# Performance work log

Measured on AMD Instinct MI355X. Metric: run time of the kernel, lower is better.

## Reference

```python
import jax, jax.numpy as jnp
import numpy as np

D_MODEL = 2048
NUM_HEADS = 16
HEAD_DIM = 128
BATCH = 4
SEQ = 2048


def setup_inputs() -> dict:
    key = jax.random.key(0)
    ks = jax.random.split(key, 5)
    s = 0.02
    return {
        "x": jax.random.normal(ks[0], (BATCH, SEQ, D_MODEL), dtype=jnp.float32),
        "Wq": jax.random.normal(ks[1], (NUM_HEADS * HEAD_DIM, D_MODEL), dtype=jnp.float32) * s,
        "Wk": jax.random.normal(ks[2], (NUM_HEADS * HEAD_DIM, D_MODEL), dtype=jnp.float32) * s,
        "Wv": jax.random.normal(ks[3], (NUM_HEADS * HEAD_DIM, D_MODEL), dtype=jnp.float32) * s,
        "Wo": jax.random.normal(ks[4], (D_MODEL, NUM_HEADS * HEAD_DIM), dtype=jnp.float32) * s,
    }


def _split_heads(t):
    b, s, _ = t.shape
    return t.reshape(b, s, NUM_HEADS, HEAD_DIM).transpose(0, 2, 1, 3)  # [b,h,s,d]


def reference(x, Wq, Wk, Wv, Wo):
    # prefill: QKV proj + causal SDPA + output proj. torch Linear: x @ W.T
    q = _split_heads(x @ Wq.T)
    k = _split_heads(x @ Wk.T)
    v = _split_heads(x @ Wv.T)
    scale = 1.0 / jnp.sqrt(jnp.asarray(HEAD_DIM, dtype=x.dtype))
    scores = jnp.einsum("bhqd,bhkd->bhqk", q, k) * scale
    causal = jnp.tril(jnp.ones((SEQ, SEQ), dtype=bool))
    scores = jnp.where(causal, scores, jnp.finfo(scores.dtype).min)
    attn = jax.nn.softmax(scores, axis=-1)
    y = jnp.einsum("bhqk,bhkd->bhqd", attn, v)
    y = y.transpose(0, 2, 1, 3).reshape(x.shape[0], SEQ, NUM_HEADS * HEAD_DIM)
    y = y @ Wo.T
    return (y, k, v)
```

## Files before the change

kernel.cpp:

```cpp
#include <hip/hip_runtime.h>
#include <stdint.h>

#define DM 2048
#define NH 16
#define HD 128
#define BB 4
#define SS 2048
#define BS (BB*SS)
#define NQKV (3*DM)
#define SCQ 0.12751744565f

typedef __bf16 bf16_t;
typedef __attribute__((ext_vector_type(8))) __bf16 bf16x8;
typedef __attribute__((ext_vector_type(4))) float f32x4;
typedef __attribute__((ext_vector_type(16))) float f32x16;
typedef __attribute__((ext_vector_type(4))) float float4v;
typedef __attribute__((ext_vector_type(4))) unsigned int uint4v;
typedef __attribute__((ext_vector_type(4))) unsigned short ushort4v;
typedef __attribute__((ext_vector_type(8))) unsigned short ushort8;

__device__ __forceinline__ unsigned short f2bf(float f) {
  unsigned u = __float_as_uint(f);
  u += 0x7fffu + ((u >> 16) & 1u);
  return (unsigned short)(u >> 16);
}

__device__ __forceinline__ void gl16(const void* g, void* l) {
  __builtin_amdgcn_global_load_lds(
      (const __attribute__((address_space(1))) unsigned int*)(unsigned long long)g,
      (__attribute__((address_space(3))) unsigned int*)(unsigned int)(unsigned long long)l,
      16, 0, 0);
}

#define DSR(dst, addr, IMM)                                                   \
  asm volatile("ds_read_b128 %0, %1 offset:" IMM : "=v"(dst) : "v"(addr))

__global__ void conv_all(const float* __restrict__ x,  const float* __restrict__ wq,
                         const float* __restrict__ wk, const float* __restrict__ wv,
                         const float* __restrict__ wo,
                         unsigned short* __restrict__ xbf,
                         unsigned short* __restrict__ wqkv,
                         unsigned short* __restrict__ wobf) {
  const int NX = BS * DM / 4;
  const int NW = DM * DM / 4;
  int i = blockIdx.x * blockDim.x + threadIdx.x;
  int stride = gridDim.x * blockDim.x;
  for (; i < NX + 4 * NW; i += stride) {
    const float4v* src;
    ushort4v* dst;
    if (i < NX)               { src = (const float4v*)x  + i;            dst = (ushort4v*)xbf + i; }
    else if (i < NX + NW)     { int j = i - NX;          src = (const float4v*)wq + j; dst = (ushort4v*)wqkv + j; }
    else if (i < NX + 2 * NW) { int j = i - NX - NW;     src = (const float4v*)wk + j; dst = (ushort4v*)wqkv + NW + j; }
    else if (i < NX + 3 * NW) { int j = i - NX - 2 * NW; src = (const float4v*)wv + j; dst = (ushort4v*)wqkv + 2 * NW + j; }
    else                      { int j = i - NX - 3 * NW; src = (const float4v*)wo + j; dst = (ushort4v*)wobf + j; }
    float4v v = *src;
    ushort4v o;
    o.x = f2bf(v.x); o.y = f2bf(v.y); o.z = f2bf(v.z); o.w = f2bf(v.w);
    *dst = o;
  }
}

__global__ void vtrans(const float* __restrict__ vf, bf16_t* __restrict__ vt) {
  __shared__ unsigned short T[128 * 64];
  const int t = threadIdx.x;
  const int s0 = blockIdx.x * 64;
  const int bh = blockIdx.y;
  const size_t in_off = (size_t)bh * SS * HD;
  const int sr = t >> 5, c4 = t & 31;
#pragma unroll
  for (int j = 0; j < 8; ++j) {
    int s = j * 8 + sr;
    float4v v = *(const float4v*)(vf + in_off + (size_t)(s0 + s) * HD + c4 * 4);
#pragma unroll
    for (int q = 0; q < 4; ++q) {
      int d = c4 * 4 + q;
      int bc = s * 2;
      int byt = d * 128 + ((((bc >> 4) ^ (d & 7)) << 4) | (bc & 15));
      *(unsigned short*)((char*)T + byt) = f2bf(v[q]);
    }
  }
  __syncthreads();
  const int dr = t >> 3, c8 = t & 7;
  unsigned short* out = (unsigned short*)vt + (size_t)bh * HD * SS;
#pragma unroll
  for (int j = 0; j < 4; ++j) {
    int d = j * 32 + dr;
    ushort8 val = *(const ushort8*)((char*)T + d * 128 + ((c8 ^ (d & 7)) << 4));
    *(ushort8*)(out + (size_t)d * SS + s0 + c8 * 8) = val;
  }
}

__global__ void gemmq(const bf16_t* __restrict__ A, const bf16_t* __restrict__ Bm,
                      bf16_t* __restrict__ qbf, bf16_t* __restrict__ kbt,
                      float* __restrict__ kf, float* __restrict__ vf) {
  __shared__ bf16_t As[128 * 64];
  __shared__ bf16_t Bs[128 * 64];
  const int t = threadIdx.x;
  const int w = t >> 6, lane = t & 63;
  const int wm = (w >> 1) * 64, wn = (w & 1) * 64;
  const int row0 = blockIdx.x * 128, col0 = blockIdx.y * 128;
  const int fr = lane & 15, fq = lane >> 4;
  const int K = DM;

  f32x4 acc[4][4] = {};

  for (int kk = 0; kk < K; kk += 64) {
    __syncthreads();
#pragma unroll
    for (int j = 0; j < 4; ++j) {
      int u = j * 256 + t;
      int r = u >> 3, c = u & 7;
      uint4v dA = *(const uint4v*)(A + (size_t)(row0 + r) * K + kk + c * 8);
      uint4v dB = *(const uint4v*)(Bm + (size_t)(col0 + r) * K + kk + c * 8);
      int so = r * 64 + ((c ^ ((r >> 1) & 7)) * 8);
      *(uint4v*)(As + so) = dA;
      *(uint4v*)(Bs + so) = dB;
    }
    __syncthreads();
#pragma unroll
    for (int ks = 0; ks < 2; ++ks) {
      bf16x8 af[4], bfv[4];
#pragma unroll
      for (int f = 0; f < 4; ++f) {
        int ra = wm + f * 16 + fr;
        af[f] = *(const bf16x8*)(As + ra * 64 + (((fq + ks * 4) ^ ((ra >> 1) & 7)) * 8));
        int rb = wn + f * 16 + fr;
        bfv[f] = *(const bf16x8*)(Bs + rb * 64 + (((fq + ks * 4) ^ ((rb >> 1) & 7)) * 8));
      }
#pragma unroll
      for (int i = 0; i < 4; ++i)
#pragma unroll
        for (int jn = 0; jn < 4; ++jn)
          acc[i][jn] = __builtin_amdgcn_mfma_f32_16x16x32_bf16(af[i], bfv[jn], acc[i][jn], 0, 0, 0);
    }
  }

#pragma unroll
  for (int i = 0; i < 4; ++i) {
#pragma unroll
    for (int jn = 0; jn < 4; ++jn) {
#pragma unroll
      for (int r = 0; r < 4; ++r) {
        int m = row0 + wm + i * 16 + fq * 4 + r;
        int n = col0 + wn + jn * 16 + fr;
        float v = acc[i][jn][r];
        int b = m >> 11, s = m & 2047;
        if (n < DM) {
          int h = n >> 7, d = n & 127;
          qbf[(((size_t)(b * NH + h)) * SS + s) * HD + d] = (bf16_t)(v * SCQ);
        } else if (n < 2 * DM) {
          int nn = n - DM, h = nn >> 7, d = nn & 127;
          size_t o = (((size_t)(b * NH + h)) * SS + s) * HD + d;
          kbt[o] = (bf16_t)v;
          kf[o] = v;
        } else {
          int nn = n - 2 * DM, h = nn >> 7, d = nn & 127;
          vf[(((size_t)(b * NH + h)) * SS + s) * HD + d] = v;
        }
      }
    }
  }
}

template<int MODE>
__global__ __launch_bounds__(512)
void gemmr4(const bf16_t* __restrict__ A, const bf16_t* __restrict__ Bm,
            const int K, const int N, const int nbx,
            float* __restrict__ Cf) {
  __shared__ bf16_t As[4][256 * 32];
  __shared__ bf16_t Bs[4][256 * 32];
  const int t = threadIdx.x, w = t >> 6, lane = t & 63;
  const int fr = lane & 15, fq = lane >> 4;
  const int cpx = gridDim.x >> 3;
  const int orig = blockIdx.x;
  const int wg = (orig & 7) * cpx + (orig >> 3);
  const int bm = wg % nbx, bn = wg / nbx;
  const int row0 = bm * 256, col0 = bn * 256;
  const int wm = (w >> 2) * 128, wn = (w & 3) * 64;

  const bf16_t* Asrc[2];
  const bf16_t* Bsrc[2];
  int dst[2];
#pragma unroll
  for (int j = 0; j < 2; ++j) {
    int u = j * 512 + t, r = u >> 2, c = u & 3;
    Asrc[j] = A + (size_t)(row0 + r) * K + ((c ^ ((r >> 1) & 3)) * 8);
    Bsrc[j] = Bm + (size_t)(col0 + r) * K + ((c ^ ((r >> 1) & 3)) * 8);
    dst[j] = u * 16;
  }
  const int NT = K >> 5;
  f32x4 acc[8][4] = {};

  const unsigned As0 = (unsigned)(unsigned long long)(const void*)&As[0][0];
  const unsigned Bs0 = (unsigned)(unsigned long long)(const void*)&Bs[0][0];
  const unsigned xorc = (unsigned)((fq ^ ((fr >> 1) & 3)) << 4);
  const unsigned aoff = (unsigned)((wm + fr) * 64) + xorc;
  const unsigned boff = (unsigned)((wn + fr) * 64) + xorc;

#define STAGE(TT)                                                  \
  {                                                                \
    const int sl_ = (TT) & 3;                                      \
    const size_t ko_ = (size_t)(TT) * 32;                          \
    gl16(Asrc[0] + ko_, (char*)(&As[sl_][0]) + dst[0]);            \
    gl16(Asrc[1] + ko_, (char*)(&As[sl_][0]) + dst[1]);            \
    gl16(Bsrc[0] + ko_, (char*)(&Bs[sl_][0]) + dst[0]);            \
    gl16(Bsrc[1] + ko_, (char*)(&Bs[sl_][0]) + dst[1]);            \
  }

#define MFQUAD(FI, AV)                                                        \
  acc[FI][0] = __builtin_amdgcn_mfma_f32_16x16x32_bf16(                       \
      __builtin_bit_cast(bf16x8, AV), __builtin_bit_cast(bf16x8, bv0), acc[FI][0], 0, 0, 0); \
  acc[FI][1] = __builtin_amdgcn_mfma_f32_16x16x32_bf16(                       \
      __builtin_bit_cast(bf16x8, AV), __builtin_bit_cast(bf16x8, bv1), acc[FI][1], 0, 0, 0); \
  acc[FI][2] = __builtin_amdgcn_mfma_f32_16x16x32_bf16(                       \
      __builtin_bit_cast(bf16x8, AV), __builtin_bit_cast(bf16x8, bv2), acc[FI][2], 0, 0, 0); \
  acc[FI][3] = __builtin_amdgcn_mfma_f32_16x16x32_bf16(                       \
      __builtin_bit_cast(bf16x8, AV), __builtin_bit_cast(bf16x8, bv3), acc[FI][3], 0, 0, 0);

  STAGE(0); STAGE(1); STAGE(2);

  for (int T = 0; T < NT; ++T) {
    if (T + 2 < NT) {
      asm volatile("s_waitcnt vmcnt(8)" ::: "memory");
    } else if (T + 1 < NT) {
      asm volatile("s_waitcnt vmcnt(4)" ::: "memory");
    } else {
      asm volatile("s_waitcnt vmcnt(0)" ::: "memory");
    }
    asm volatile("s_barrier" ::: "memory");
    if (T + 3 < NT) STAGE(T + 3);

    const unsigned ab = As0 + (unsigned)(T & 3) * 16384 + aoff;
    const unsigned bb = Bs0 + (unsigned)(T & 3) * 16384 + boff;
    uint4v bv0, bv1, bv2, bv3, a0, a1, a2, a3, a4, a5, a6, a7;
    DSR(bv0, bb, "0");    DSR(bv1, bb, "1024");
    DSR(bv2, bb, "2048"); DSR(bv3, bb, "3072");
    DSR(a0, ab, "0");     DSR(a1, ab, "1024");
    DSR(a2, ab, "2048");  DSR(a3, ab, "3072");
    DSR(a4, ab, "4096");  DSR(a5, ab, "5120");
    DSR(a6, ab, "6144");  DSR(a7, ab, "7168");

    asm volatile("s_waitcnt lgkmcnt(4)" ::: "memory");
    __builtin_amdgcn_sched_barrier(0);
    __builtin_amdgcn_s_setprio(1);
    MFQUAD(0, a0) MFQUAD(1, a1) MFQUAD(2, a2) MFQUAD(3, a3)
    __builtin_amdgcn_s_setprio(0);

    asm volatile("s_waitcnt lgkmcnt(0)" ::: "memory");
    __builtin_amdgcn_sched_barrier(0);
    __builtin_amdgcn_s_setprio(1);
    MFQUAD(4, a4) MFQUAD(5, a5) MFQUAD(6, a6) MFQUAD(7, a7)
    __builtin_amdgcn_s_setprio(0);
  }
#undef STAGE
#undef MFQUAD

#pragma unroll
  for (int f = 0; f < 8; ++f) {
#pragma unroll
    for (int jn = 0; jn < 4; ++jn) {
#pragma unroll
      for (int r = 0; r < 4; ++r) {
        int m = row0 + wm + f * 16 + fq * 4 + r;
        int n = col0 + wn + jn * 16 + fr;
        Cf[(size_t)m * N + n] = acc[f][jn][r];
      }
    }
  }
}

__global__ __launch_bounds__(256, 2)
void attn_fwd5(const bf16_t* __restrict__ qbf, const bf16_t* __restrict__ kbf,
               const bf16_t* __restrict__ vt, bf16_t* __restrict__ aout) {
  __shared__ bf16_t Ks[2][64 * 128];
  __shared__ bf16_t Vs[2][64 * 128];
  const int t = threadIdx.x, w = t >> 6, lane = t & 63;
  const int l31 = lane & 31, hi = lane >> 5;
  const int orig = blockIdx.x;
  const int wg = (orig & 7) * 128 + (orig >> 3);
  const int bh = wg >> 4;
  const int qt = 15 - (wg & 15);
  const int q0 = qt * 128;
  const int nt = 2 * qt + 2;
  const size_t bh_off = (size_t)bh * SS * HD;
  const char* kbase = (const char*)(kbf + bh_off);
  const char* vbase = (const char*)(vt + bh_off);

  const char* ksrc[4];
  const char* vsrc[4];
#pragma unroll
  for (int i = 0; i < 4; ++i) {
    int r = (w * 4 + i) * 4 + (lane >> 4);
    int c = (lane & 15) ^ (r & 15);
    ksrc[i] = kbase + r * 256 + c * 16;
    int d = 2 * r + (c >> 3);
    vsrc[i] = vbase + (size_t)d * (SS * 2) + (c & 7) * 16;
  }

  bf16x8 qfr[8];
  {
    const char* qrow = (const char*)(qbf + bh_off + (size_t)(q0 + w * 32 + l31) * HD);
#pragma unroll
    for (int ds = 0; ds < 8; ++ds)
      qfr[ds] = *(const bf16x8*)(qrow + ds * 32 + hi * 16);
  }

#pragma unroll
  for (int i = 0; i < 4; ++i) {
    gl16(ksrc[i], (char*)(&Ks[0][0]) + (w * 4 + i) * 1024);
    gl16(vsrc[i], (char*)(&Vs[0][0]) + (w * 4 + i) * 1024);
    ksrc[i] += 16384;
    vsrc[i] += 128;
  }

  float mrow = -3.0e38f, lrow = 0.f;
  f32x16 accO[4] = {};

  auto make_pa = [&](const f32x16& sv, bf16x8& paA, bf16x8& paB) {
    unsigned W[8];
#pragma unroll
    for (int m = 0; m < 8; ++m) {
      float lo = sv[2 * m], hh = sv[2 * m + 1];
      asm("v_cvt_pk_bf16_f32 %0, %1, %2" : "=v"(W[m]) : "v"(lo), "v"(hh));
    }
    asm volatile("v_permlane32_swap_b32 %0, %1" : "+v"(W[0]), "+v"(W[2]));
    asm volatile("v_permlane32_swap_b32 %0, %1" : "+v"(W[1]), "+v"(W[3]));
    asm volatile("v_permlane32_swap_b32 %0, %1" : "+v"(W[4]), "+v"(W[6]));
    asm volatile("v_permlane32_swap_b32 %0, %1" : "+v"(W[5]), "+v"(W[7]));
    uint4v u0; u0.x = W[0]; u0.y = W[1]; u0.z = W[2]; u0.w = W[3];
    paA = __builtin_bit_cast(bf16x8, u0);
    uint4v u1; u1.x = W[4]; u1.y = W[5]; u1.z = W[6]; u1.w = W[7];
    paB = __builtin_bit_cast(bf16x8, u1);
  };

  for (int kt = 0; kt < nt; ++kt) {
    const int cur = kt & 1;
    __syncthreads();

    if (kt + 1 < nt) {
#pragma unroll
      for (int i = 0; i < 4; ++i) {
        gl16(ksrc[i], (char*)(&Ks[cur ^ 1][0]) + (w * 4 + i) * 1024);
        gl16(vsrc[i], (char*)(&Vs[cur ^ 1][0]) + (w * 4 + i) * 1024);
        ksrc[i] += 16384;
        vsrc[i] += 128;
      }
    }

    const char* kl = (const char*)&Ks[cur][0];
    f32x16 s0 = {}, s1 = {};
    const int rck = l31 & 15;
    __builtin_amdgcn_s_setprio(1);
#pragma unroll
    for (int ds = 0; ds < 8; ++ds) {
      int ch = ((2 * ds + hi) ^ rck) << 4;
      bf16x8 kf0 = *(const bf16x8*)(kl + l31 * 256 + ch);
      s0 = __builtin_amdgcn_mfma_f32_32x32x16_bf16(kf0, qfr[ds], s0, 0, 0, 0);
      bf16x8 kf1 = *(const bf16x8*)(kl + (32 + l31) * 256 + ch);
      s1 = __builtin_amdgcn_mfma_f32_32x32x16_bf16(kf1, qfr[ds], s1, 0, 0, 0);
    }
    __builtin_amdgcn_s_setprio(0);

    const int kv0 = kt * 64;
    if (kt >= 2 * qt) {
      const int qg = q0 + w * 32 + l31;
#pragma unroll
      for (int r = 0; r < 16; ++r) {
        int klo = kv0 + (r & 3) + 8 * (r >> 2) + 4 * hi;
        if (klo > qg) s0[r] = -3.0e38f;
        if (klo + 32 > qg) s1[r] = -3.0e38f;
      }
    }
    float rm = s0[0];
#pragma unroll
    for (int r = 1; r < 16; ++r) rm = fmaxf(rm, s0[r]);
#pragma unroll
    for (int r = 0; r < 16; ++r) rm = fmaxf(rm, s1[r]);
    rm = fmaxf(rm, __shfl_xor(rm, 32, 64));
    if (__ballot(rm > mrow + 8.0f)) {
      float mnew = fmaxf(mrow, rm);
      float fct = __builtin_amdgcn_exp2f(mrow - mnew);
      mrow = mnew;
      lrow *= fct;
#pragma unroll
      for (int r = 0; r < 16; ++r) {
        float f = __shfl(fct, (r & 3) + 8 * (r >> 2) + 4 * hi, 64);
        accO[0][r] *= f; accO[1][r] *= f; accO[2][r] *= f; accO[3][r] *= f;
      }
    }
    float ss = 0.f;
#pragma unroll
    for (int r = 0; r < 16; ++r) { float p = __builtin_amdgcn_exp2f(s0[r] - mrow); s0[r] = p; ss += p; }
#pragma unroll
    for (int r = 0; r < 16; ++r) { float p = __builtin_amdgcn_exp2f(s1[r] - mrow); s1[r] = p; ss += p; }
    ss += __shfl_xor(ss, 32, 64);
    lrow += ss;

    bf16x8 pa00, pa01, pa10, pa11;
    make_pa(s0, pa00, pa01);
    make_pa(s1, pa10, pa11);

    const char* vl = (const char*)&Vs[cur][0];
    __builtin_amdgcn_s_setprio(1);
#pragma unroll
    for (int dt = 0; dt < 4; ++dt) {
      int R = dt * 16 + (l31 >> 1);
      int cb = (l31 & 1) << 3;
      int rx = R & 15;
      bf16x8 v00 = *(const bf16x8*)(vl + R * 256 + (((cb + 0 + hi) ^ rx) << 4));
      accO[dt] = __builtin_amdgcn_mfma_f32_32x32x16_bf16(pa00, v00, accO[dt], 0, 0, 0);
      bf16x8 v01 = *(const bf16x8*)(vl + R * 256 + (((cb + 2 + hi) ^ rx) << 4));
      accO[dt] = __builtin_amdgcn_mfma_f32_32x32x16_bf16(pa01, v01, accO[dt], 0, 0, 0);
      bf16x8 v10 = *(const bf16x8*)(vl + R * 256 + (((cb + 4 + hi) ^ rx) << 4));
      accO[dt] = __builtin_amdgcn_mfma_f32_32x32x16_bf16(pa10, v10, accO[dt], 0, 0, 0);
      bf16x8 v11 = *(const bf16x8*)(vl + R * 256 + (((cb + 6 + hi) ^ rx) << 4));
      accO[dt] = __builtin_amdgcn_mfma_f32_32x32x16_bf16(pa11, v11, accO[dt], 0, 0, 0);
    }
    __builtin_amdgcn_s_setprio(0);
  }

  const int b = bh >> 4, h = bh & 15;
#pragma unroll
  for (int r = 0; r < 16; ++r) {
    int qr = (r & 3) + 8 * (r >> 2) + 4 * hi;
    float inv = __builtin_amdgcn_rcpf(__shfl(lrow, qr, 64));
    int srow = q0 + w * 32 + qr;
    bf16_t* orow = aout + ((size_t)(b * SS + srow)) * DM + h * HD + l31;
    orow[0]  = (bf16_t)(accO[0][r] * inv);
    orow[32] = (bf16_t)(accO[1][r] * inv);
    orow[64] = (bf16_t)(accO[2][r] * inv);
    orow[96] = (bf16_t)(accO[3][r] * inv);
  }
}

extern "C" void kernel_launch(void* const* d_in, const int* in_sizes, int n_in,
                              void* d_out, int out_size, void* d_ws, size_t ws_size,
                              hipStream_t stream) {
  (void)in_sizes; (void)n_in; (void)out_size; (void)ws_size;
  const float* x  = (const float*)d_in[0];
  const float* Wq = (const float*)d_in[1];
  const float* Wk = (const float*)d_in[2];
  const float* Wv = (const float*)d_in[3];
  const float* Wo = (const float*)d_in[4];

  float* y  = (float*)d_out;
  float* kf = y + (size_t)BS * DM;
  float* vf = kf + (size_t)BS * DM;

  char* ws = (char*)d_ws;
  bf16_t* xbf  = (bf16_t*)ws;
  bf16_t* abf  = xbf;
  bf16_t* qbf  = (bf16_t*)(ws + (size_t)32 * 1024 * 1024);
  bf16_t* wqkv = (bf16_t*)(ws + (size_t)64 * 1024 * 1024);
  bf16_t* wobf = (bf16_t*)(ws + (size_t)88 * 1024 * 1024);
  bf16_t* kbt  = (bf16_t*)y;
  bf16_t* vtb  = (bf16_t*)((char*)y + (size_t)32 * 1024 * 1024);

  conv_all<<<2048, 256, 0, stream>>>(x, Wq, Wk, Wv, Wo,
                                     (unsigned short*)xbf, (unsigned short*)wqkv,
                                     (unsigned short*)wobf);

  gemmq<<<dim3(BS / 128, NQKV / 128), 256, 0, stream>>>(xbf, wqkv, qbf, kbt, kf, vf);

  vtrans<<<dim3(SS / 64, BB * NH), 256, 0, stream>>>(vf, vtb);

  attn_fwd5<<<1024, 256, 0, stream>>>(qbf, kbt, vtb, abf);

  gemmr4<0><<<256, 512, 0, stream>>>(abf, wobf, DM, DM, 32, y);
}
```

Measured before the change: 454.3 us.

## Double-buffer QKV GEMM tiles with direct global-to-LDS loads

The QKV projection GEMM now keeps two LDS buffers for A and B and prefetches the next K-tile with direct global-to-LDS loads (gl16) while the MFMAs run on the current tile. The XOR swizzle moves from the LDS store address to the global source address, so a contiguous LDS destination stays compatible with the existing swizzled fragment reads. This is meant to hide global-load latency and remove the register round-trip and one barrier per iteration. In exchange it doubles LDS use, which may lower occupancy, and correctness depends on gl16 completing before the next barrier.

```diff
diff --git a/kernel.cpp b/kernel.cpp
--- a/kernel.cpp
+++ b/kernel.cpp
@@ -93,39 +93,59 @@
 __global__ void gemmq(const bf16_t* __restrict__ A, const bf16_t* __restrict__ Bm,
                       bf16_t* __restrict__ qbf, bf16_t* __restrict__ kbt,
                       float* __restrict__ kf, float* __restrict__ vf) {
-  __shared__ bf16_t As[128 * 64];
-  __shared__ bf16_t Bs[128 * 64];
+  __shared__ bf16_t As[2][128 * 64];
+  __shared__ bf16_t Bs[2][128 * 64];
   const int t = threadIdx.x;
   const int w = t >> 6, lane = t & 63;
   const int wm = (w >> 1) * 64, wn = (w & 1) * 64;
   const int row0 = blockIdx.x * 128, col0 = blockIdx.y * 128;
   const int fr = lane & 15, fq = lane >> 4;
   const int K = DM;
+  const int NT = K >> 6;
+
+  const bf16_t* Asrc[4];
+  const bf16_t* Bsrc[4];
+  int dst[4];
+#pragma unroll
+  for (int j = 0; j < 4; ++j) {
+    int u = j * 256 + t, r = u >> 3, c = u & 7;
+    Asrc[j] = A + (size_t)(row0 + r) * K + ((c ^ ((r >> 1) & 7)) * 8);
+    Bsrc[j] = Bm + (size_t)(col0 + r) * K + ((c ^ ((r >> 1) & 7)) * 8);
+    dst[j] = u * 16;
+  }
 
   f32x4 acc[4][4] = {};
 
-  for (int kk = 0; kk < K; kk += 64) {
+#pragma unroll
+  for (int j = 0; j < 4; ++j) {
+    gl16(Asrc[j], (char*)(&As[0][0]) + dst[j]);
+    gl16(Bsrc[j], (char*)(&Bs[0][0]) + dst[j]);
+  }
+
+  for (int T = 0; T < NT; ++T) {
+    const int cur = T & 1;
     __syncthreads();
-#pragma unroll
-    for (int j = 0; j < 4; ++j) {
-      int u = j * 256 + t;
-      int r = u >> 3, c = u & 7;
-      uint4v dA = *(const uint4v*)(A + (size_t)(row0 + r) * K + kk + c * 8);
-      uint4v dB = *(const uint4v*)(Bm + (size_t)(col0 + r) * K + kk + c * 8);
-      int so = r * 64 + ((c ^ ((r >> 1) & 7)) * 8);
-      *(uint4v*)(As + so) = dA;
-      *(uint4v*)(Bs + so) = dB;
-    }
-    __syncthreads();
+
+    if (T + 1 < NT) {
+      const size_t ko = (size_t)(T + 1) * 64;
+#pragma unroll
+      for (int j = 0; j < 4; ++j) {
+        gl16(Asrc[j] + ko, (char*)(&As[cur ^ 1][0]) + dst[j]);
+        gl16(Bsrc[j] + ko, (char*)(&Bs[cur ^ 1][0]) + dst[j]);
+      }
+    }
+
+    const bf16_t* al = &As[cur][0];
+    const bf16_t* bl = &Bs[cur][0];
 #pragma unroll
     for (int ks = 0; ks < 2; ++ks) {
       bf16x8 af[4], bfv[4];
 #pragma unroll
       for (int f = 0; f < 4; ++f) {
         int ra = wm + f * 16 + fr;
-        af[f] = *(const bf16x8*)(As + ra * 64 + (((fq + ks * 4) ^ ((ra >> 1) & 7)) * 8));
+        af[f] = *(const bf16x8*)(al + ra * 64 + (((fq + ks * 4) ^ ((ra >> 1) & 7)) * 8));
         int rb = wn + f * 16 + fr;
-        bfv[f] = *(const bf16x8*)(Bs + rb * 64 + (((fq + ks * 4) ^ ((rb >> 1) & 7)) * 8));
+        bfv[f] = *(const bf16x8*)(bl + rb * 64 + (((fq + ks * 4) ^ ((rb >> 1) & 7)) * 8));
       }
 #pragma unroll
       for (int i = 0; i < 4; ++i)
```

Result: no change. 448.3 us (-1.3%).
